# Performance work log

Hardware: AMD Instinct MI355X
Metric: run time of the kernel (lower is better)

The kernel has to match this reference:

```python
import jax, jax.numpy as jnp
import numpy as np

N, E = 10000, 320000
H, NH, ED = 128, 8, 32
HD = H // NH
FF = 4 * H


def _layer_norm(x, g, b, eps=1e-5):
    m = jnp.mean(x, axis=-1, keepdims=True)
    v = jnp.mean((x - m) ** 2, axis=-1, keepdims=True)
    return (x - m) / jnp.sqrt(v + eps) * g + b


def setup_inputs() -> dict:
    key = jax.random.key(0)
    ks = jax.random.split(key, 16)
    def p(k, shape, fan_in):
        return jax.random.normal(k, shape, jnp.float32) * (fan_in ** -0.5)
    return {
        "x": jax.random.normal(ks[0], (N, H), jnp.float32),
        "edge_index": jax.random.randint(ks[1], (2, E), 0, N, dtype=jnp.int32).astype(jnp.int64),
        "edge_attr": jax.random.normal(ks[2], (E, ED), jnp.float32),
        "Wq": p(ks[3], (H, H), H), "bq": jnp.zeros((H,), jnp.float32),
        "Wk": p(ks[4], (H, H), H), "bk": jnp.zeros((H,), jnp.float32),
        "Wv": p(ks[5], (H, H), H), "bv": jnp.zeros((H,), jnp.float32),
        "We": p(ks[6], (ED, NH), ED), "be": jnp.zeros((NH,), jnp.float32),
        "Wo": p(ks[7], (H, H), H), "bo": jnp.zeros((H,), jnp.float32),
        "ln1_g": jnp.ones((H,), jnp.float32), "ln1_b": jnp.zeros((H,), jnp.float32),
        "W1": p(ks[8], (H, FF), H), "b1": jnp.zeros((FF,), jnp.float32),
        "W2": p(ks[9], (FF, H), FF), "b2": jnp.zeros((H,), jnp.float32),
        "ln2_g": jnp.ones((H,), jnp.float32), "ln2_b": jnp.zeros((H,), jnp.float32),
    }


def reference(x, edge_index, edge_attr, Wq, bq, Wk, bk, Wv, bv, We, be,
              Wo, bo, ln1_g, ln1_b, W1, b1, W2, b2, ln2_g, ln2_b):
    n = x.shape[0]
    src, dst = edge_index[0], edge_index[1]
    # node projections -> [N, NH, HD]
    q = (x @ Wq + bq).reshape(n, NH, HD)
    k = (x @ Wk + bk).reshape(n, NH, HD)
    v = (x @ Wv + bv).reshape(n, NH, HD)
    # per-edge scores [E, NH] with edge-conditioned bias
    edge_bias = edge_attr @ We + be
    scores = jnp.sum(q[src] * k[dst], axis=-1) / jnp.sqrt(jnp.float32(HD)) + edge_bias
    # scatter-softmax over edges grouped by dst
    mx = jax.ops.segment_max(scores, dst, num_segments=n)
    ex = jnp.exp(scores - mx[dst])
    den = jax.ops.segment_sum(ex, dst, num_segments=n)
    attn = ex / (den[dst] + 1e-8)  # [E, NH]
    # weighted scatter-add of source values
    agg = jax.ops.segment_sum(v[src] * attn[..., None], dst, num_segments=n)  # [N, NH, HD]
    out = agg.reshape(n, H) @ Wo + bo
    x = _layer_norm(x + out, ln1_g, ln1_b)
    h = jax.nn.gelu(x @ W1 + b1, approximate=False) @ W2 + b2
    return _layer_norm(x + h, ln2_g, ln2_b)
```

## Files before the change

### kernel.cpp

```cpp
#include <hip/hip_runtime.h>
#include <hip/hip_bf16.h>

#define HH    128
#define NHEAD 8
#define HDIM  16
#define EDIM  32
#define FFDIM 512
#define BM    16
#define CHUNK 16

__global__ __launch_bounds__(512)
void qkv_kernel(const float* __restrict__ x,
                const float* __restrict__ Wq, const float* __restrict__ bq,
                const float* __restrict__ Wk, const float* __restrict__ bk,
                const float* __restrict__ Wv, const float* __restrict__ bv,
                float* __restrict__ q, float* __restrict__ k, float* __restrict__ v,
                int* __restrict__ cnt, int* __restrict__ cursor)
{
    const int row0 = blockIdx.x * BM;
    const int t  = threadIdx.x;
    const int rg = t >> 7;
    const int c  = t & 127;
    __shared__ float xs[BM * HH];

    if (t < BM)                cnt[row0 + t] = 0;
    else if (t < 2 * BM)       cursor[row0 + (t - BM)] = 0;
    *(float4*)&xs[t * 4] = *(const float4*)&x[(size_t)row0 * HH + t * 4];
    __syncthreads();

    float aq[4] = {0.f, 0.f, 0.f, 0.f};
    float ak[4] = {0.f, 0.f, 0.f, 0.f};
    float av[4] = {0.f, 0.f, 0.f, 0.f};
    for (int i0 = 0; i0 < HH; i0 += 4) {
        float4 xr[4];
        #pragma unroll
        for (int r = 0; r < 4; ++r)
            xr[r] = *(const float4*)&xs[(4 * rg + r) * HH + i0];
        #pragma unroll
        for (int u = 0; u < 4; ++u) {
            float wq = Wq[(i0 + u) * HH + c];
            float wk = Wk[(i0 + u) * HH + c];
            float wv = Wv[(i0 + u) * HH + c];
            #pragma unroll
            for (int r = 0; r < 4; ++r) {
                float xv = ((const float*)&xr[r])[u];
                aq[r] += xv * wq;  ak[r] += xv * wk;  av[r] += xv * wv;
            }
        }
    }
    float bqv = bq[c], bkv = bk[c], bvv = bv[c];
    #pragma unroll
    for (int r = 0; r < 4; ++r) {
        size_t o = (size_t)(row0 + 4 * rg + r) * HH + c;
        q[o] = aq[r] + bqv;
        k[o] = ak[r] + bkv;
        v[o] = av[r] + bvv;
    }
}

__global__ void hist_kernel(const int* __restrict__ ei, int E, int* __restrict__ cnt)
{
    int e = blockIdx.x * 256 + threadIdx.x;
    if (e < E) atomicAdd(&cnt[ei[E + e]], 1);
}

#define SCAN_T 1024
__global__ __launch_bounds__(SCAN_T)
void scan_kernel(const int* __restrict__ cnt, int n, int* __restrict__ rowptr)
{
    __shared__ int part[SCAN_T];
    const int t = threadIdx.x;
    const int per = (n + SCAN_T - 1) / SCAN_T;
    const int beg = t * per;
    const int end = min(beg + per, n);
    int sum = 0;
    for (int i = beg; i < end; ++i) sum += cnt[i];
    part[t] = sum;
    __syncthreads();
    for (int off = 1; off < SCAN_T; off <<= 1) {
        int vv = (t >= off) ? part[t - off] : 0;
        __syncthreads();
        part[t] += vv;
        __syncthreads();
    }
    int base = (t == 0) ? 0 : part[t - 1];
    for (int i = beg; i < end; ++i) { rowptr[i] = base; base += cnt[i]; }
    if (t == SCAN_T - 1) rowptr[n] = base;
}

__global__ __launch_bounds__(256)
void scatter_kernel(const int* __restrict__ ei, int E,
                    const float* __restrict__ ea,
                    const float* __restrict__ We, const float* __restrict__ be,
                    const int* __restrict__ rowptr, int* __restrict__ cursor,
                    int* __restrict__ csr_src, float* __restrict__ csr_eb)
{
    __shared__ float wsh[EDIM * NHEAD];
    __shared__ float bsh[NHEAD];
    const int t = threadIdx.x;
    if (t < EDIM * NHEAD) wsh[t] = We[t];
    if (t < NHEAD) bsh[t] = be[t];
    __syncthreads();
    int e = blockIdx.x * 256 + t;
    if (e >= E) return;
    int src = ei[e], dst = ei[E + e];
    int slot = rowptr[dst] + atomicAdd(&cursor[dst], 1);
    csr_src[slot] = src;
    float eb[NHEAD];
    #pragma unroll
    for (int h = 0; h < NHEAD; ++h) eb[h] = bsh[h];
    const float* eap = ea + (size_t)e * EDIM;
    #pragma unroll
    for (int j0 = 0; j0 < EDIM; j0 += 4) {
        float4 a = *(const float4*)&eap[j0];
        #pragma unroll
        for (int h = 0; h < NHEAD; ++h) {
            eb[h] += a.x * wsh[(j0    ) * NHEAD + h]
                   + a.y * wsh[(j0 + 1) * NHEAD + h]
                   + a.z * wsh[(j0 + 2) * NHEAD + h]
                   + a.w * wsh[(j0 + 3) * NHEAD + h];
        }
    }
    #pragma unroll
    for (int h = 0; h < NHEAD; ++h) csr_eb[(size_t)slot * NHEAD + h] = eb[h];
}

__global__ __launch_bounds__(128)
void edge_kernel(const float* __restrict__ q, const float* __restrict__ k,
                 const float* __restrict__ v,
                 const int* __restrict__ rowptr,
                 const int* __restrict__ csr_src, const float* __restrict__ csr_eb,
                 float* __restrict__ agg)
{
    const int node = blockIdx.x;
    const int t = threadIdx.x;
    const int c = t >> 3, h = t & 7;
    const int f = t, fh = t >> 4;
    __shared__ float ks[HH];
    __shared__ float sraw[CHUNK][NHEAD];
    __shared__ float p[CHUNK][NHEAD];
    __shared__ int   ssrc[CHUNK];
    __shared__ float m[NHEAD], dn[NHEAD], fac[NHEAD];

    ks[t] = k[(size_t)node * HH + t];
    if (t < NHEAD) { m[t] = -3.0e38f; dn[t] = 0.f; }
    const int beg = rowptr[node], end = rowptr[node + 1];
    float acc = 0.f;
    __syncthreads();

    for (int b0 = beg; b0 < end; b0 += CHUNK) {
        const int C = min(CHUNK, end - b0);
        float sc = -3.0e38f;
        if (c < C) {
            int src = csr_src[b0 + c];
            if (h == 0) ssrc[c] = src;
            const float* qp = q + (size_t)src * HH + h * HDIM;
            float d0 = 0.f;
            #pragma unroll
            for (int d = 0; d < HDIM; d += 4) {
                float4 qv = *(const float4*)&qp[d];
                d0 += qv.x * ks[h * HDIM + d]     + qv.y * ks[h * HDIM + d + 1]
                    + qv.z * ks[h * HDIM + d + 2] + qv.w * ks[h * HDIM + d + 3];
            }
            sc = d0 * 0.25f + csr_eb[(size_t)(b0 + c) * NHEAD + h];
        }
        sraw[c][h] = sc;
        __syncthreads();
        if (t < NHEAD) {
            float mo = m[t], mc = -3.0e38f;
            #pragma unroll 4
            for (int cc = 0; cc < CHUNK; ++cc) mc = fmaxf(mc, sraw[cc][t]);
            float mn = fmaxf(mo, mc);
            float fa = __expf(mo - mn);
            float s = 0.f;
            #pragma unroll 4
            for (int cc = 0; cc < CHUNK; ++cc) {
                float pe = __expf(sraw[cc][t] - mn);
                p[cc][t] = pe;  s += pe;
            }
            dn[t] = dn[t] * fa + s;
            m[t] = mn;  fac[t] = fa;
        }
        __syncthreads();
        acc *= fac[fh];
        for (int cc = 0; cc < C; ++cc)
            acc += p[cc][fh] * v[(size_t)ssrc[cc] * HH + f];
        __syncthreads();
    }
    agg[(size_t)node * HH + f] = acc / (dn[fh] + 1e-8f);
}

__global__ __launch_bounds__(256)
void tail_kernel(const float* __restrict__ x, const float* __restrict__ agg,
                 const float* __restrict__ Wo, const float* __restrict__ bo,
                 const float* __restrict__ l1g, const float* __restrict__ l1b,
                 const float* __restrict__ W1, const float* __restrict__ b1,
                 const float* __restrict__ W2, const float* __restrict__ b2,
                 const float* __restrict__ l2g, const float* __restrict__ l2b,
                 float* __restrict__ out)
{
    const int row0 = blockIdx.x * BM;
    const int t  = threadIdx.x;
    const int rg = t >> 7;
    const int c  = t & 127;
    const int wh = (t >> 6) & 1;
    const int rbase = 8 * rg;

    __shared__ float xs[BM * HH];
    __shared__ float hs[BM * FFDIM];
    __shared__ float redS[4][8], redS2[4][8];

    *(float4*)&xs[t * 8]     = *(const float4*)&agg[(size_t)row0 * HH + t * 8];
    *(float4*)&xs[t * 8 + 4] = *(const float4*)&agg[(size_t)row0 * HH + t * 8 + 4];
    __syncthreads();

    float y[8] = {0.f, 0.f, 0.f, 0.f, 0.f, 0.f, 0.f, 0.f};
    for (int i0 = 0; i0 < HH; i0 += 4) {
        float4 xr[8];
        #pragma unroll
        for (int r = 0; r < 8; ++r)
            xr[r] = *(const float4*)&xs[(rbase + r) * HH + i0];
        #pragma unroll
        for (int u = 0; u < 4; ++u) {
            float w = Wo[(size_t)(i0 + u) * HH + c];
            #pragma unroll
            for (int r = 0; r < 8; ++r) y[r] += ((const float*)&xr[r])[u] * w;
        }
    }
    {
        float bov = bo[c];
        #pragma unroll
        for (int r = 0; r < 8; ++r)
            y[r] += bov + x[(size_t)(row0 + rbase + r) * HH + c];
    }

    float s[8], s2[8];
    #pragma unroll
    for (int r = 0; r < 8; ++r) { s[r] = y[r]; s2[r] = y[r] * y[r]; }
    #pragma unroll
    for (int off = 32; off > 0; off >>= 1) {
        #pragma unroll
        for (int r = 0; r < 8; ++r) {
            s[r]  += __shfl_down(s[r],  off);
            s2[r] += __shfl_down(s2[r], off);
        }
    }
    if ((t & 63) == 0) {
        #pragma unroll
        for (int r = 0; r < 8; ++r) {
            redS [rg * 2 + wh][r] = s[r];
            redS2[rg * 2 + wh][r] = s2[r];
        }
    }
    __syncthreads();
    float x1v[8];
    {
        float g1 = l1g[c], bb1 = l1b[c];
        #pragma unroll
        for (int r = 0; r < 8; ++r) {
            float ssum = redS [rg * 2][r] + redS [rg * 2 + 1][r];
            float ssq  = redS2[rg * 2][r] + redS2[rg * 2 + 1][r];
            float mean = ssum * (1.0f / HH);
            float var  = ssq  * (1.0f / HH) - mean * mean;
            x1v[r] = (y[r] - mean) * rsqrtf(var + 1e-5f) * g1 + bb1;
        }
    }
    #pragma unroll
    for (int r = 0; r < 8; ++r) xs[(rbase + r) * HH + c] = x1v[r];
    __syncthreads();

    float h[8][4];
    #pragma unroll
    for (int r = 0; r < 8; ++r)
        #pragma unroll
        for (int kk = 0; kk < 4; ++kk) h[r][kk] = 0.f;
    for (int i0 = 0; i0 < HH; i0 += 4) {
        float4 xr[8];
        #pragma unroll
        for (int r = 0; r < 8; ++r)
            xr[r] = *(const float4*)&xs[(rbase + r) * HH + i0];
        #pragma unroll
        for (int u = 0; u < 4; ++u) {
            const float* wrow = &W1[(size_t)(i0 + u) * FFDIM + c];
            float w0 = wrow[0], w1 = wrow[128], w2 = wrow[256], w3 = wrow[384];
            #pragma unroll
            for (int r = 0; r < 8; ++r) {
                float xu = ((const float*)&xr[r])[u];
                h[r][0] += xu * w0;  h[r][1] += xu * w1;
                h[r][2] += xu * w2;  h[r][3] += xu * w3;
            }
        }
    }
    {
        float b10 = b1[c], b11 = b1[c + 128], b12 = b1[c + 256], b13 = b1[c + 384];
        #pragma unroll
        for (int r = 0; r < 8; ++r) {
            float a0 = h[r][0] + b10, a1 = h[r][1] + b11;
            float a2 = h[r][2] + b12, a3 = h[r][3] + b13;
            float* hrow = &hs[(rbase + r) * FFDIM + c];
            hrow[0]   = 0.5f * a0 * (1.0f + erff(a0 * 0.70710678118f));
            hrow[128] = 0.5f * a1 * (1.0f + erff(a1 * 0.70710678118f));
            hrow[256] = 0.5f * a2 * (1.0f + erff(a2 * 0.70710678118f));
            hrow[384] = 0.5f * a3 * (1.0f + erff(a3 * 0.70710678118f));
        }
    }
    __syncthreads();

    float y2[8] = {0.f, 0.f, 0.f, 0.f, 0.f, 0.f, 0.f, 0.f};
    for (int j0 = 0; j0 < FFDIM; j0 += 4) {
        float4 hr[8];
        #pragma unroll
        for (int r = 0; r < 8; ++r)
            hr[r] = *(const float4*)&hs[(rbase + r) * FFDIM + j0];
        #pragma unroll
        for (int u = 0; u < 4; ++u) {
            float w = W2[(size_t)(j0 + u) * HH + c];
            #pragma unroll
            for (int r = 0; r < 8; ++r) y2[r] += ((const float*)&hr[r])[u] * w;
        }
    }
    {
        float b2v = b2[c];
        #pragma unroll
        for (int r = 0; r < 8; ++r) y2[r] += b2v + x1v[r];
    }

    #pragma unroll
    for (int r = 0; r < 8; ++r) { s[r] = y2[r]; s2[r] = y2[r] * y2[r]; }
    #pragma unroll
    for (int off = 32; off > 0; off >>= 1) {
        #pragma unroll
        for (int r = 0; r < 8; ++r) {
            s[r]  += __shfl_down(s[r],  off);
            s2[r] += __shfl_down(s2[r], off);
        }
    }
    if ((t & 63) == 0) {
        #pragma unroll
        for (int r = 0; r < 8; ++r) {
            redS [rg * 2 + wh][r] = s[r];
            redS2[rg * 2 + wh][r] = s2[r];
        }
    }
    __syncthreads();
    {
        float g2 = l2g[c], bb2 = l2b[c];
        #pragma unroll
        for (int r = 0; r < 8; ++r) {
            float ssum = redS [rg * 2][r] + redS [rg * 2 + 1][r];
            float ssq  = redS2[rg * 2][r] + redS2[rg * 2 + 1][r];
            float mean = ssum * (1.0f / HH);
            float var  = ssq  * (1.0f / HH) - mean * mean;
            out[(size_t)(row0 + rbase + r) * HH + c] =
                (y2[r] - mean) * rsqrtf(var + 1e-5f) * g2 + bb2;
        }
    }
}

extern "C" void kernel_launch(void* const* d_in, const int* in_sizes, int n_in,
                              void* d_out, int out_size, void* d_ws, size_t ws_size,
                              hipStream_t stream)
{
    const float* x   = (const float*)d_in[0];
    const int*   ei  = (const int*)d_in[1];
    const float* ea  = (const float*)d_in[2];
    const float* Wq  = (const float*)d_in[3];
    const float* bq  = (const float*)d_in[4];
    const float* Wk  = (const float*)d_in[5];
    const float* bk  = (const float*)d_in[6];
    const float* Wv  = (const float*)d_in[7];
    const float* bv  = (const float*)d_in[8];
    const float* We  = (const float*)d_in[9];
    const float* be  = (const float*)d_in[10];
    const float* Wo  = (const float*)d_in[11];
    const float* bo  = (const float*)d_in[12];
    const float* l1g = (const float*)d_in[13];
    const float* l1b = (const float*)d_in[14];
    const float* W1  = (const float*)d_in[15];
    const float* b1  = (const float*)d_in[16];
    const float* W2  = (const float*)d_in[17];
    const float* b2  = (const float*)d_in[18];
    const float* l2g = (const float*)d_in[19];
    const float* l2b = (const float*)d_in[20];
    float* out = (float*)d_out;

    const int n = in_sizes[0] / HH;
    const int E = in_sizes[1] / 2;

    float* ws      = (float*)d_ws;
    float* q       = ws;
    float* k       = q       + (size_t)n * HH;
    float* v       = k       + (size_t)n * HH;
    float* csr_eb  = v       + (size_t)n * HH;
    float* agg     = csr_eb  + (size_t)E * NHEAD;
    int*   cnt     = (int*)(agg + (size_t)n * HH);
    int*   cursor  = cnt     + n;
    int*   rowptr  = cursor  + n;
    int*   csr_src = rowptr  + (n + 1);

    qkv_kernel<<<n / BM, 512, 0, stream>>>(x, Wq, bq, Wk, bk, Wv, bv,
                                           q, k, v, cnt, cursor);
    hist_kernel<<<(E + 255) / 256, 256, 0, stream>>>(ei, E, cnt);
    scan_kernel<<<1, SCAN_T, 0, stream>>>(cnt, n, rowptr);
    scatter_kernel<<<(E + 255) / 256, 256, 0, stream>>>(ei, E, ea, We, be,
                                                        rowptr, cursor,
                                                        csr_src, csr_eb);
    edge_kernel<<<n, 128, 0, stream>>>(q, k, v, rowptr, csr_src, csr_eb, agg);
    tail_kernel<<<n / BM, 256, 0, stream>>>(x, agg, Wo, bo, l1g, l1b,
                                            W1, b1, W2, b2, l2g, l2b, out);
}
```

Before: 315.9 us.

## Widen edge kernel to 256 threads with split aggregation; halve tail row tile

The edge kernel now runs 256 threads per node. It scores 32 edges per chunk and splits the weighted V accumulation across two halves of the block, then reduces them through shared memory. The softmax loops bound to the actual chunk size instead of the full chunk width. The tail kernel processes 8 rows per block instead of 16, doubling the block count for more occupancy at the cost of reusing each weight load across fewer rows.

```diff
diff --git a/kernel.cpp b/kernel.cpp
--- a/kernel.cpp
+++ b/kernel.cpp
@@ -7,7 +7,8 @@
 #define EDIM  32
 #define FFDIM 512
 #define BM    16
-#define CHUNK 16
+#define BMT   8
+#define CHK   32
 
 __global__ __launch_bounds__(512)
 void qkv_kernel(const float* __restrict__ x,
@@ -125,7 +126,7 @@
     for (int h = 0; h < NHEAD; ++h) csr_eb[(size_t)slot * NHEAD + h] = eb[h];
 }
 
-__global__ __launch_bounds__(128)
+__global__ __launch_bounds__(256)
 void edge_kernel(const float* __restrict__ q, const float* __restrict__ k,
                  const float* __restrict__ v,
                  const int* __restrict__ rowptr,
@@ -135,21 +136,23 @@
     const int node = blockIdx.x;
     const int t = threadIdx.x;
     const int c = t >> 3, h = t & 7;
-    const int f = t, fh = t >> 4;
+    const int f = t & 127, half = t >> 7;
+    const int fh = f >> 4;
     __shared__ float ks[HH];
-    __shared__ float sraw[CHUNK][NHEAD];
-    __shared__ float p[CHUNK][NHEAD];
-    __shared__ int   ssrc[CHUNK];
+    __shared__ float sraw[CHK][NHEAD];
+    __shared__ float p[CHK][NHEAD];
+    __shared__ int   ssrc[CHK];
     __shared__ float m[NHEAD], dn[NHEAD], fac[NHEAD];
-
-    ks[t] = k[(size_t)node * HH + t];
+    __shared__ float accs[2][HH];
+
+    if (t < HH) ks[t] = k[(size_t)node * HH + t];
     if (t < NHEAD) { m[t] = -3.0e38f; dn[t] = 0.f; }
     const int beg = rowptr[node], end = rowptr[node + 1];
     float acc = 0.f;
     __syncthreads();
 
-    for (int b0 = beg; b0 < end; b0 += CHUNK) {
-        const int C = min(CHUNK, end - b0);
+    for (int b0 = beg; b0 < end; b0 += CHK) {
+        const int C = min(CHK, end - b0);
         float sc = -3.0e38f;
         if (c < C) {
             int src = csr_src[b0 + c];
@@ -168,13 +171,11 @@
         __syncthreads();
         if (t < NHEAD) {
             float mo = m[t], mc = -3.0e38f;
-            #pragma unroll 4
-            for (int cc = 0; cc < CHUNK; ++cc) mc = fmaxf(mc, sraw[cc][t]);
+            for (int cc = 0; cc < C; ++cc) mc = fmaxf(mc, sraw[cc][t]);
             float mn = fmaxf(mo, mc);
             float fa = __expf(mo - mn);
             float s = 0.f;
-            #pragma unroll 4
-            for (int cc = 0; cc < CHUNK; ++cc) {
+            for (int cc = 0; cc < C; ++cc) {
                 float pe = __expf(sraw[cc][t] - mn);
                 p[cc][t] = pe;  s += pe;
             }
@@ -183,11 +184,16 @@
         }
         __syncthreads();
         acc *= fac[fh];
-        for (int cc = 0; cc < C; ++cc)
+        const int lim = min(half * 16 + 16, C);
+        for (int cc = half * 16; cc < lim; ++cc)
             acc += p[cc][fh] * v[(size_t)ssrc[cc] * HH + f];
         __syncthreads();
     }
-    agg[(size_t)node * HH + f] = acc / (dn[fh] + 1e-8f);
+    accs[half][f] = acc;
+    __syncthreads();
+    if (t < HH)
+        agg[(size_t)node * HH + t] =
+            (accs[0][t] + accs[1][t]) / (dn[t >> 4] + 1e-8f);
 }
 
 __global__ __launch_bounds__(256)
@@ -199,65 +205,64 @@
                  const float* __restrict__ l2g, const float* __restrict__ l2b,
                  float* __restrict__ out)
 {
-    const int row0 = blockIdx.x * BM;
+    const int row0 = blockIdx.x * BMT;
     const int t  = threadIdx.x;
     const int rg = t >> 7;
     const int c  = t & 127;
     const int wh = (t >> 6) & 1;
-    const int rbase = 8 * rg;
-
-    __shared__ float xs[BM * HH];
-    __shared__ float hs[BM * FFDIM];
-    __shared__ float redS[4][8], redS2[4][8];
-
-    *(float4*)&xs[t * 8]     = *(const float4*)&agg[(size_t)row0 * HH + t * 8];
-    *(float4*)&xs[t * 8 + 4] = *(const float4*)&agg[(size_t)row0 * HH + t * 8 + 4];
-    __syncthreads();
-
-    float y[8] = {0.f, 0.f, 0.f, 0.f, 0.f, 0.f, 0.f, 0.f};
+    const int rbase = 4 * rg;
+
+    __shared__ float xs[BMT * HH];
+    __shared__ float hs[BMT * FFDIM];
+    __shared__ float redS[4][4], redS2[4][4];
+
+    *(float4*)&xs[t * 4] = *(const float4*)&agg[(size_t)row0 * HH + t * 4];
+    __syncthreads();
+
+    float y[4] = {0.f, 0.f, 0.f, 0.f};
     for (int i0 = 0; i0 < HH; i0 += 4) {
-        float4 xr[8];
-        #pragma unroll
-        for (int r = 0; r < 8; ++r)
+        float4 xr[4];
+        #pragma unroll
+        for (int r = 0; r < 4; ++r)
             xr[r] = *(const float4*)&xs[(rbase + r) * HH + i0];
         #pragma unroll
         for (int u = 0; u < 4; ++u) {
             float w = Wo[(size_t)(i0 + u) * HH + c];
             #pragma unroll
-            for (int r = 0; r < 8; ++r) y[r] += ((const float*)&xr[r])[u] * w;
+            for (int r = 0; r < 4; ++r) y[r] += ((const float*)&xr[r])[u] * w;
         }
     }
     {
         float bov = bo[c];
         #pragma unroll
-        for (int r = 0; r < 8; ++r)
+        for (int r = 0; r < 4; ++r)
             y[r] += bov + x[(size_t)(row0 + rbase + r) * HH + c];
     }
 
-    float s[8], s2[8];
-    #pragma unroll
-    for (int r = 0; r < 8; ++r) { s[r] = y[r]; s2[r] = y[r] * y[r]; }
+    float s[4], s2[4];
+    #pragma unroll
+    for (int r = 0; r < 4; ++r) { s[r] = y[r]; s2[r] = y[r] * y[r]; }
     #pragma unroll
     for (int off = 32; off > 0; off >>= 1) {
         #pragma unroll
-        for (int r = 0; r < 8; ++r) {
+        for (int r = 0; r < 4; ++r) {
             s[r]  += __shfl_down(s[r],  off);
             s2[r] += __shfl_down(s2[r], off);
         }
     }
     if ((t & 63) == 0) {
         #pragma unroll
-        for (int r = 0; r < 8; ++r) {
+        for (int r = 0; r < 4; ++r) {
             redS [rg * 2 + wh][r] = s[r];
             redS2[rg * 2 + wh][r] = s2[r];
         }
     }
     __syncthreads();
-    float x1v[8];
+    float x1v[4];
     {
         float g1 = l1g[c], bb1 = l1b[c];
         #pragma unroll
-        for (int r = 0; r < 8; ++r) {
+        for (int r = 0; r < 4; ++r) {
             float ssum = redS [rg * 2][r] + redS [rg * 2 + 1][r];
             float ssq  = redS2[rg * 2][r] + redS2[rg * 2 + 1][r];
             float mean = ssum * (1.0f / HH);
@@ -266,25 +271,25 @@
         }
     }
     #pragma unroll
-    for (int r = 0; r < 8; ++r) xs[(rbase + r) * HH + c] = x1v[r];
-    __syncthreads();
-
-    float h[8][4];
-    #pragma unroll
-    for (int r = 0; r < 8; ++r)
+    for (int r = 0; r < 4; ++r) xs[(rbase + r) * HH + c] = x1v[r];
+    __syncthreads();
+
+    float h[4][4];
+    #pragma unroll
+    for (int r = 0; r < 4; ++r)
         #pragma unroll
         for (int kk = 0; kk < 4; ++kk) h[r][kk] = 0.f;
     for (int i0 = 0; i0 < HH; i0 += 4) {
-        float4 xr[8];
-        #pragma unroll
-        for (int r = 0; r < 8; ++r)
+        float4 xr[4];
+        #pragma unroll
+        for (int r = 0; r < 4; ++r)
             xr[r] = *(const float4*)&xs[(rbase + r) * HH + i0];
         #pragma unroll
         for (int u = 0; u < 4; ++u) {
             const float* wrow = &W1[(size_t)(i0 + u) * FFDIM + c];
             float w0 = wrow[0], w1 = wrow[128], w2 = wrow[256], w3 = wrow[384];
             #pragma unroll
-            for (int r = 0; r < 8; ++r) {
+            for (int r = 0; r < 4; ++r) {
                 float xu = ((const float*)&xr[r])[u];
                 h[r][0] += xu * w0;  h[r][1] += xu * w1;
                 h[r][2] += xu * w2;  h[r][3] += xu * w3;
@@ -294,7 +299,7 @@
     {
         float b10 = b1[c], b11 = b1[c + 128], b12 = b1[c + 256], b13 = b1[c + 384];
         #pragma unroll
-        for (int r = 0; r < 8; ++r) {
+        for (int r = 0; r < 4; ++r) {
             float a0 = h[r][0] + b10, a1 = h[r][1] + b11;
             float a2 = h[r][2] + b12, a3 = h[r][3] + b13;
             float* hrow = &hs[(rbase + r) * FFDIM + c];
@@ -306,38 +311,38 @@
     }
     __syncthreads();
 
-    float y2[8] = {0.f, 0.f, 0.f, 0.f, 0.f, 0.f, 0.f, 0.f};
+    float y2[4] = {0.f, 0.f, 0.f, 0.f};
     for (int j0 = 0; j0 < FFDIM; j0 += 4) {
-        float4 hr[8];
-        #pragma unroll
-        for (int r = 0; r < 8; ++r)
+        float4 hr[4];
+        #pragma unroll
+        for (int r = 0; r < 4; ++r)
             hr[r] = *(const float4*)&hs[(rbase + r) * FFDIM + j0];
         #pragma unroll
         for (int u = 0; u < 4; ++u) {
             float w = W2[(size_t)(j0 + u) * HH + c];
             #pragma unroll
-            for (int r = 0; r < 8; ++r) y2[r] += ((const float*)&hr[r])[u] * w;
+            for (int r = 0; r < 4; ++r) y2[r] += ((const float*)&hr[r])[u] * w;
         }
     }
     {
         float b2v = b2[c];
         #pragma unroll
-        for (int r = 0; r < 8; ++r) y2[r] += b2v + x1v[r];
-    }
-
-    #pragma unroll
-    for (int r = 0; r < 8; ++r) { s[r] = y2[r]; s2[r] = y2[r] * y2[r]; }
+        for (int r = 0; r < 4; ++r) y2[r] += b2v + x1v[r];
+    }
+
+    #pragma unroll
+    for (int r = 0; r < 4; ++r) { s[r] = y2[r]; s2[r] = y2[r] * y2[r]; }
     #pragma unroll
     for (int off = 32; off > 0; off >>= 1) {
         #pragma unroll
-        for (int r = 0; r < 8; ++r) {
+        for (int r = 0; r < 4; ++r) {
             s[r]  += __shfl_down(s[r],  off);
             s2[r] += __shfl_down(s2[r], off);
         }
     }
     if ((t & 63) == 0) {
         #pragma unroll
-        for (int r = 0; r < 8; ++r) {
+        for (int r = 0; r < 4; ++r) {
             redS [rg * 2 + wh][r] = s[r];
             redS2[rg * 2 + wh][r] = s2[r];
         }
@@ -346,7 +351,7 @@
     {
         float g2 = l2g[c], bb2 = l2b[c];
         #pragma unroll
-        for (int r = 0; r < 8; ++r) {
+        for (int r = 0; r < 4; ++r) {
             float ssum = redS [rg * 2][r] + redS [rg * 2 + 1][r];
             float ssq  = redS2[rg * 2][r] + redS2[rg * 2 + 1][r];
             float mean = ssum * (1.0f / HH);
@@ -405,7 +410,7 @@
     scatter_kernel<<<(E + 255) / 256, 256, 0, stream>>>(ei, E, ea, We, be,
                                                         rowptr, cursor,
                                                         csr_src, csr_eb);
-    edge_kernel<<<n, 128, 0, stream>>>(q, k, v, rowptr, csr_src, csr_eb, agg);
-    tail_kernel<<<n / BM, 256, 0, stream>>>(x, agg, Wo, bo, l1g, l1b,
-                                            W1, b1, W2, b2, l2g, l2b, out);
-}
+    edge_kernel<<<n, 256, 0, stream>>>(q, k, v, rowptr, csr_src, csr_eb, agg);
+    tail_kernel<<<n / BMT, 256, 0, stream>>>(x, agg, Wo, bo, l1g, l1b,
+                                             W1, b1, W2, b2, l2g, l2b, out);
+}
```

New measurement: 341.6 us. 8.1% more time.
